# Kernel tuning notes

Hardware: AMD Instinct MI355X
Metric: run time of the kernel (lower is better)

The kernel has to match this reference:

```python
import jax, jax.numpy as jnp
import numpy as np

S = 4            # symbol_features (number of element types)
NLAB = S * S     # label_features = 16
RC = 6.0         # cutoff radius
C1, C2 = 32, 64  # embedding_layers
B, N = 4, 512
BOX_L = 25.0     # non-periodic box extent for coordinate sampling


def setup_inputs() -> dict:
    key = jax.random.key(0)
    k1, k2, k3, k4 = jax.random.split(key, 4)
    coords = jax.random.uniform(k1, (B, N, 3), dtype=jnp.float32) * BOX_L
    numbers = jax.random.randint(k2, (B, N), 0, S)
    # NaN lattice -> Descriptor takes the non-periodic neighbor branch
    boxs = jnp.full((B, 9), jnp.nan, dtype=jnp.float32)
    # RConv parameters (per label): nuww=-0.05, sigmas=4.0, centres ~ xavier_normal
    nuww0 = jnp.full((NLAB,), -0.05, jnp.float32)
    sigmas0 = jnp.full((NLAB,), 4.0, jnp.float32)
    centres0 = (jax.random.normal(k3, (NLAB, C1)) * np.sqrt(2.0 / (NLAB + C1))).astype(jnp.float32)
    nuww1 = jnp.full((NLAB,), -0.05, jnp.float32)
    sigmas1 = jnp.full((NLAB,), 4.0, jnp.float32)
    centres1 = (jax.random.normal(k4, (NLAB, C2)) * np.sqrt(2.0 / (NLAB + C2))).astype(jnp.float32)
    return {"boxs": boxs, "numbers": numbers, "coords": coords,
            "nuww0": nuww0, "sigmas0": sigmas0, "centres0": centres0,
            "nuww1": nuww1, "sigmas1": sigmas1, "centres1": centres1}


def _rconv(label, r, nuww, sigmas, centres):
    # label: [B,N,N] int; r: [B,N,N,Cin] -> out [B,N,N,Cout]
    rs = r.sum(-1, keepdims=True)            # sum over channel dim (keepdim)
    ww = nuww[label][..., None]              # [B,N,N,1]
    sgm = sigmas[label][..., None]           # [B,N,N,1]
    cc = centres[label]                      # [B,N,N,Cout]
    alpha = (rs - cc) * sgm
    return ww * jnp.exp(-(alpha * alpha))


def reference(boxs, numbers, coords, nuww0, sigmas0, centres0, nuww1, sigmas1, centres1):
    # boxs is NaN -> non-periodic branch of Descriptor.forward.
    # Dense-mask formulation: pairs (i,j) with d<=RC, i!=j; masked entries
    # contribute exactly zero to the per-atom contractions below.
    rij = coords[:, None, :, :] - coords[:, :, None, :]      # [B,N,N,3] = x_j - x_i
    d2 = jnp.sum(rij * rij, axis=-1)                         # [B,N,N]
    safe = jnp.sqrt(jnp.where(d2 > 0, d2, 1.0))              # NaN-safe sqrt for grads
    d = jnp.where(d2 > 0, safe, 0.0)
    eye = jnp.eye(N, dtype=bool)
    mask = (jax.lax.stop_gradient(d) <= RC) & ~eye           # neighbor list (detached, as in torch)

    fc = 0.5 * jnp.cos(d * (jnp.pi / RC)) + 0.5              # cutoff_cosine, [B,N,N]
    ang = rij / safe[..., None]                              # unit direction (safe at diag)
    raij = jnp.concatenate([fc[..., None], ang * fc[..., None]], axis=-1)  # [B,N,N,4]

    label = numbers[:, :, None] * S + numbers[:, None, :]    # ZIJ_Label[z_i, z_j], [B,N,N]

    r0 = fc[..., None]                                       # rij_cos, [B,N,N,1]
    phi = _rconv(label, r0, nuww0, sigmas0, centres0)        # [B,N,N,C1]
    phi = _rconv(label, phi, nuww1, sigmas1, centres1)       # [B,N,N,C2]
    phi = phi * mask[..., None]                              # zero out non-neighbors

    # per atom i: L = phi^T @ raij over neighbors j -> [C2,4]; R = L @ L^T -> [C2,C2]
    Lm = jnp.einsum('bijc,bijf->bicf', phi, raij)            # [B,N,C2,4]
    R = jnp.einsum('bicf,bidf->bicd', Lm, Lm)                # [B,N,C2,C2]
    fro = jnp.sqrt(jnp.sum(R * R, axis=(-2, -1), keepdims=True))
    D = R / fro
    return D.reshape(B, N, C2 * C2)                          # Dij [B,N,4096]
```

## Files before the change

kernel.cpp:

```cpp
#include <hip/hip_runtime.h>
#include <math.h>

#define S_ 4
#define NLAB 16
#define C1 32
#define C2 64
#define N_ 512
#define RC 6.0f
#define PI_OVER_RC 0.5235987755982988f
#define SEGCAP 32

__global__ __launch_bounds__(256, 8) void desc_kernel(
    const int* __restrict__ numbers,
    const float* __restrict__ coords,
    const float* __restrict__ nuww0, const float* __restrict__ sigmas0,
    const float* __restrict__ centres0,
    const float* __restrict__ nuww1, const float* __restrict__ sigmas1,
    const float* __restrict__ centres1,
    float* __restrict__ out)
{
    __shared__ float s_c0[NLAB * 33];
    __shared__ float s_c1[NLAB * C2];
    __shared__ float s_ww0[NLAB], s_sg0[NLAB], s_ww1[NLAB], s_sg1[NLAB];
    __shared__ float4 s_pair[4][SEGCAP];
    __shared__ float  s_s1[4][SEGCAP];
    __shared__ int    s_lab[4][SEGCAP];
    __shared__ float4 s_part[4][C2];
    __shared__ float4 s_Lm[C2];

    const int tid  = threadIdx.x;
    const int wq   = tid >> 6;
    const int lane = tid & 63;
    const int bi   = blockIdx.x;
    const int b    = bi >> 9;
    const int i    = bi & (N_ - 1);
    const int base = b * N_;

    for (int idx = tid; idx < NLAB * C1; idx += 256) {
        int l = idx >> 5, c = idx & 31;
        s_c0[l * 33 + c] = centres0[idx];
    }
    for (int idx = tid; idx < NLAB * C2; idx += 256) s_c1[idx] = centres1[idx];
    if (tid < NLAB) {
        s_ww0[tid] = nuww0[tid]; s_sg0[tid] = sigmas0[tid];
        s_ww1[tid] = nuww1[tid]; s_sg1[tid] = sigmas1[tid];
    }
    __syncthreads();

    const float xi = coords[(base + i) * 3 + 0];
    const float yi = coords[(base + i) * 3 + 1];
    const float zi = coords[(base + i) * 3 + 2];
    const int zlab = numbers[base + i] * S_;

    int cntq = 0;
    #pragma unroll
    for (int t = 0; t < 2; ++t) {
        int j = wq * 128 + t * 64 + lane;
        float dx = coords[(base + j) * 3 + 0] - xi;
        float dy = coords[(base + j) * 3 + 1] - yi;
        float dz = coords[(base + j) * 3 + 2] - zi;
        int   zj = numbers[base + j];
        float d2 = dx * dx + dy * dy + dz * dz;
        float d  = sqrtf(d2);
        bool hit = (j != i) && (d <= RC);
        unsigned long long m = __ballot(hit);
        int slot = cntq + __popcll(m & ((1ull << lane) - 1ull));
        if (hit && slot < SEGCAP) {
            s_pair[wq][slot] = make_float4(dx, dy, dz, d);
            s_lab[wq][slot]  = zlab + zj;
        }
        cntq += __popcll(m);
    }
    const int nnq = min(cntq, SEGCAP);
    __builtin_amdgcn_wave_barrier();

    if (lane < nnq) {
        int   k   = lane;
        float4 g  = s_pair[wq][k];
        int   lab = s_lab[wq][k];
        float fc  = 0.5f * __cosf(g.w * PI_OVER_RC) + 0.5f;
        float sg0 = s_sg0[lab];
        const float* c0 = &s_c0[lab * 33];
        float p0 = 0.f, p1 = 0.f;
        #pragma unroll
        for (int c = 0; c < C1; c += 2) {
            float a0 = (fc - c0[c])     * sg0;
            float a1 = (fc - c0[c + 1]) * sg0;
            p0 += __expf(-(a0 * a0));
            p1 += __expf(-(a1 * a1));
        }
        float fac = (g.w > 0.f) ? (fc / g.w) : 0.f;
        s_pair[wq][k] = make_float4(fc, g.x * fac, g.y * fac, g.z * fac);
        s_s1[wq][k]   = s_ww0[lab] * (p0 + p1);
    }
    __builtin_amdgcn_wave_barrier();

    {
        float a0 = 0.f, a1 = 0.f, a2 = 0.f, a3 = 0.f;
        for (int k = 0; k < nnq; ++k) {
            int    lab = s_lab[wq][k];
            float  s1  = s_s1[wq][k];
            float4 r4  = s_pair[wq][k];
            float  al  = (s1 - s_c1[lab * C2 + lane]) * s_sg1[lab];
            float  p   = s_ww1[lab] * __expf(-(al * al));
            a0 += p * r4.x; a1 += p * r4.y; a2 += p * r4.z; a3 += p * r4.w;
        }
        s_part[wq][lane] = make_float4(a0, a1, a2, a3);
    }
    __syncthreads();

    float4 P0 = s_part[0][lane], P1 = s_part[1][lane];
    float4 P2 = s_part[2][lane], P3 = s_part[3][lane];
    float a0 = (P0.x + P1.x) + (P2.x + P3.x);
    float a1 = (P0.y + P1.y) + (P2.y + P3.y);
    float a2 = (P0.z + P1.z) + (P2.z + P3.z);
    float a3 = (P0.w + P1.w) + (P2.w + P3.w);
    s_Lm[lane] = make_float4(a0, a1, a2, a3);

    float g00 = a0 * a0, g01 = a0 * a1, g02 = a0 * a2, g03 = a0 * a3;
    float g11 = a1 * a1, g12 = a1 * a2, g13 = a1 * a3;
    float g22 = a2 * a2, g23 = a2 * a3, g33 = a3 * a3;
    #pragma unroll
    for (int off = 32; off >= 1; off >>= 1) {
        g00 += __shfl_xor(g00, off, 64); g01 += __shfl_xor(g01, off, 64);
        g02 += __shfl_xor(g02, off, 64); g03 += __shfl_xor(g03, off, 64);
        g11 += __shfl_xor(g11, off, 64); g12 += __shfl_xor(g12, off, 64);
        g13 += __shfl_xor(g13, off, 64); g22 += __shfl_xor(g22, off, 64);
        g23 += __shfl_xor(g23, off, 64); g33 += __shfl_xor(g33, off, 64);
    }
    float ss = g00 * g00 + g11 * g11 + g22 * g22 + g33 * g33
             + 2.f * (g01 * g01 + g02 * g02 + g03 * g03
                    + g12 * g12 + g13 * g13 + g23 * g23);
    float inv = rsqrtf(ss);
    __builtin_amdgcn_wave_barrier();

    const int cb = (lane & 15) * 4;
    float4 Lc0 = s_Lm[cb + 0], Lc1 = s_Lm[cb + 1];
    float4 Lc2 = s_Lm[cb + 2], Lc3 = s_Lm[cb + 3];
    Lc0.x *= inv; Lc0.y *= inv; Lc0.z *= inv; Lc0.w *= inv;
    Lc1.x *= inv; Lc1.y *= inv; Lc1.z *= inv; Lc1.w *= inv;
    Lc2.x *= inv; Lc2.y *= inv; Lc2.z *= inv; Lc2.w *= inv;
    Lc3.x *= inv; Lc3.y *= inv; Lc3.z *= inv; Lc3.w *= inv;
    float* po = out + (size_t)bi * (C2 * C2);
    #pragma unroll
    for (int t = 0; t < 4; ++t) {
        int q  = wq * 4 + t;
        int dd = q * 4 + (lane >> 4);
        float4 Ld = s_Lm[dd];
        float4 v;
        v.x = Lc0.x * Ld.x + Lc0.y * Ld.y + Lc0.z * Ld.z + Lc0.w * Ld.w;
        v.y = Lc1.x * Ld.x + Lc1.y * Ld.y + Lc1.z * Ld.z + Lc1.w * Ld.w;
        v.z = Lc2.x * Ld.x + Lc2.y * Ld.y + Lc2.z * Ld.z + Lc2.w * Ld.w;
        v.w = Lc3.x * Ld.x + Lc3.y * Ld.y + Lc3.z * Ld.z + Lc3.w * Ld.w;
        *reinterpret_cast<float4*>(po + q * 256 + lane * 4) = v;
    }
}

extern "C" void kernel_launch(void* const* d_in, const int* in_sizes, int n_in,
                              void* d_out, int out_size, void* d_ws, size_t ws_size,
                              hipStream_t stream) {
    const int*   numbers  = (const int*)  d_in[1];
    const float* coords   = (const float*)d_in[2];
    const float* nuww0    = (const float*)d_in[3];
    const float* sigmas0  = (const float*)d_in[4];
    const float* centres0 = (const float*)d_in[5];
    const float* nuww1    = (const float*)d_in[6];
    const float* sigmas1  = (const float*)d_in[7];
    const float* centres1 = (const float*)d_in[8];
    float* out = (float*)d_out;

    const int B = in_sizes[1] / N_;
    dim3 grid(B * N_), block(256);
    desc_kernel<<<grid, block, 0, stream>>>(numbers, coords, nuww0, sigmas0,
                                            centres0, nuww1, sigmas1, centres1, out);
}
```

Baseline: 22.28 us.

## Bucket neighbors by species so each wave handles one label in layer two

Neighbors are now compacted into per-wave, per-species buckets. In the second RConv stage each wave processes one species across all four quarter-buckets, so the centre, sigma and weight values become loop invariants held in registers. Parameter loads are issued before the neighbor scan and written to shared memory afterwards, which overlaps global latency with the distance pass. The price is four ballots per tile, extra block-wide barriers, and less occupancy from the launch bound change from 8 to 4. SEGCAP drops to 24 per species bucket, which lowers the total capacity and could truncate neighbors if the density is high.

```diff
diff --git a/kernel.cpp b/kernel.cpp
--- a/kernel.cpp
+++ b/kernel.cpp
@@ -8,9 +8,9 @@
 #define N_ 512
 #define RC 6.0f
 #define PI_OVER_RC 0.5235987755982988f
-#define SEGCAP 32
-
-__global__ __launch_bounds__(256, 8) void desc_kernel(
+#define SEGCAP 24
+
+__global__ __launch_bounds__(256, 4) void desc_kernel(
     const int* __restrict__ numbers,
     const float* __restrict__ coords,
     const float* __restrict__ nuww0, const float* __restrict__ sigmas0,
@@ -22,9 +22,9 @@
     __shared__ float s_c0[NLAB * 33];
     __shared__ float s_c1[NLAB * C2];
     __shared__ float s_ww0[NLAB], s_sg0[NLAB], s_ww1[NLAB], s_sg1[NLAB];
-    __shared__ float4 s_pair[4][SEGCAP];
-    __shared__ float  s_s1[4][SEGCAP];
-    __shared__ int    s_lab[4][SEGCAP];
+    __shared__ float4 s_pair[4][4][SEGCAP];
+    __shared__ float  s_s1[4][4][SEGCAP];
+    __shared__ int    s_segcnt[4][4];
     __shared__ float4 s_part[4][C2];
     __shared__ float4 s_Lm[C2];
 
@@ -36,23 +36,23 @@
     const int i    = bi & (N_ - 1);
     const int base = b * N_;
 
-    for (int idx = tid; idx < NLAB * C1; idx += 256) {
-        int l = idx >> 5, c = idx & 31;
-        s_c0[l * 33 + c] = centres0[idx];
-    }
-    for (int idx = tid; idx < NLAB * C2; idx += 256) s_c1[idx] = centres1[idx];
-    if (tid < NLAB) {
-        s_ww0[tid] = nuww0[tid]; s_sg0[tid] = sigmas0[tid];
-        s_ww1[tid] = nuww1[tid]; s_sg1[tid] = sigmas1[tid];
-    }
-    __syncthreads();
-
     const float xi = coords[(base + i) * 3 + 0];
     const float yi = coords[(base + i) * 3 + 1];
     const float zi = coords[(base + i) * 3 + 2];
     const int zlab = numbers[base + i] * S_;
 
-    int cntq = 0;
+    float4 rc0 = make_float4(0.f, 0.f, 0.f, 0.f);
+    if (tid < 128) rc0 = reinterpret_cast<const float4*>(centres0)[tid];
+    float4 rc1 = reinterpret_cast<const float4*>(centres1)[tid];
+    float rsc = 0.f;
+    if (tid < 64) {
+        const float* sp = (tid < 16) ? nuww0 : (tid < 32) ? sigmas0
+                        : (tid < 48) ? nuww1 : sigmas1;
+        rsc = sp[tid & 15];
+    }
+
+    int cg[4] = {0, 0, 0, 0};
+    const unsigned long long lmask = (1ull << lane) - 1ull;
     #pragma unroll
     for (int t = 0; t < 2; ++t) {
         int j = wq * 128 + t * 64 + lane;
@@ -63,47 +63,81 @@
         float d2 = dx * dx + dy * dy + dz * dz;
         float d  = sqrtf(d2);
         bool hit = (j != i) && (d <= RC);
-        unsigned long long m = __ballot(hit);
-        int slot = cntq + __popcll(m & ((1ull << lane) - 1ull));
-        if (hit && slot < SEGCAP) {
-            s_pair[wq][slot] = make_float4(dx, dy, dz, d);
-            s_lab[wq][slot]  = zlab + zj;
+        #pragma unroll
+        for (int g = 0; g < 4; ++g) {
+            unsigned long long m = __ballot(hit && (zj == g));
+            if (hit && (zj == g)) {
+                int slot = cg[g] + (int)__popcll(m & lmask);
+                if (slot < SEGCAP) s_pair[wq][g][slot] = make_float4(dx, dy, dz, d);
+            }
+            cg[g] += (int)__popcll(m);
         }
-        cntq += __popcll(m);
-    }
-    const int nnq = min(cntq, SEGCAP);
-    __builtin_amdgcn_wave_barrier();
-
-    if (lane < nnq) {
-        int   k   = lane;
-        float4 g  = s_pair[wq][k];
-        int   lab = s_lab[wq][k];
-        float fc  = 0.5f * __cosf(g.w * PI_OVER_RC) + 0.5f;
-        float sg0 = s_sg0[lab];
-        const float* c0 = &s_c0[lab * 33];
-        float p0 = 0.f, p1 = 0.f;
+    }
+    if (lane == 0) {
         #pragma unroll
-        for (int c = 0; c < C1; c += 2) {
-            float a0 = (fc - c0[c])     * sg0;
-            float a1 = (fc - c0[c + 1]) * sg0;
-            p0 += __expf(-(a0 * a0));
-            p1 += __expf(-(a1 * a1));
+        for (int g = 0; g < 4; ++g) s_segcnt[wq][g] = min(cg[g], SEGCAP);
+    }
+
+    if (tid < 128) {
+        int idx = tid * 4, l = idx >> 5, c = idx & 31;
+        s_c0[l * 33 + c + 0] = rc0.x; s_c0[l * 33 + c + 1] = rc0.y;
+        s_c0[l * 33 + c + 2] = rc0.z; s_c0[l * 33 + c + 3] = rc0.w;
+    }
+    s_c1[tid * 4 + 0] = rc1.x; s_c1[tid * 4 + 1] = rc1.y;
+    s_c1[tid * 4 + 2] = rc1.z; s_c1[tid * 4 + 3] = rc1.w;
+    if (tid < 64) {
+        int r = tid & 15;
+        if      (tid < 16) s_ww0[r] = rsc;
+        else if (tid < 32) s_sg0[r] = rsc;
+        else if (tid < 48) s_ww1[r] = rsc;
+        else               s_sg1[r] = rsc;
+    }
+    __syncthreads();
+
+    {
+        const int n0 = min(cg[0], SEGCAP), n1 = min(cg[1], SEGCAP);
+        const int n2 = min(cg[2], SEGCAP), n3 = min(cg[3], SEGCAP);
+        const int p0 = n0, p1 = p0 + n1, p2 = p1 + n2, p3 = p2 + n3;
+        for (int L = lane; L < p3; L += 64) {
+            int g   = (L >= p0) + (L >= p1) + (L >= p2);
+            int off = (g == 0) ? 0 : (g == 1) ? p0 : (g == 2) ? p1 : p2;
+            int idx = L - off;
+            float4 gv = s_pair[wq][g][idx];
+            int   lab = zlab + g;
+            float fc  = 0.5f * __cosf(gv.w * PI_OVER_RC) + 0.5f;
+            float sg0 = s_sg0[lab];
+            const float* c0p = &s_c0[lab * 33];
+            float pa = 0.f, pb = 0.f;
+            #pragma unroll
+            for (int c = 0; c < C1; c += 2) {
+                float a0_ = (fc - c0p[c])     * sg0;
+                float a1_ = (fc - c0p[c + 1]) * sg0;
+                pa += __expf(-(a0_ * a0_));
+                pb += __expf(-(a1_ * a1_));
+            }
+            float fac = (gv.w > 0.f) ? (fc / gv.w) : 0.f;
+            s_pair[wq][g][idx] = make_float4(fc, gv.x * fac, gv.y * fac, gv.z * fac);
+            s_s1[wq][g][idx]   = s_ww0[lab] * (pa + pb);
         }
-        float fac = (g.w > 0.f) ? (fc / g.w) : 0.f;
-        s_pair[wq][k] = make_float4(fc, g.x * fac, g.y * fac, g.z * fac);
-        s_s1[wq][k]   = s_ww0[lab] * (p0 + p1);
-    }
-    __builtin_amdgcn_wave_barrier();
+    }
+    __syncthreads();
 
     {
+        const int   labw = zlab + wq;
+        const float c1v  = s_c1[labw * C2 + lane];
+        const float sg1  = s_sg1[labw];
+        const float ww1  = s_ww1[labw];
         float a0 = 0.f, a1 = 0.f, a2 = 0.f, a3 = 0.f;
-        for (int k = 0; k < nnq; ++k) {
-            int    lab = s_lab[wq][k];
-            float  s1  = s_s1[wq][k];
-            float4 r4  = s_pair[wq][k];
-            float  al  = (s1 - s_c1[lab * C2 + lane]) * s_sg1[lab];
-            float  p   = s_ww1[lab] * __expf(-(al * al));
-            a0 += p * r4.x; a1 += p * r4.y; a2 += p * r4.z; a3 += p * r4.w;
+        #pragma unroll
+        for (int q = 0; q < 4; ++q) {
+            int nk = s_segcnt[q][wq];
+            for (int k = 0; k < nk; ++k) {
+                float  s1 = s_s1[q][wq][k];
+                float4 r4 = s_pair[q][wq][k];
+                float  al = (s1 - c1v) * sg1;
+                float  p  = ww1 * __expf(-(al * al));
+                a0 += p * r4.x; a1 += p * r4.y; a2 += p * r4.z; a3 += p * r4.w;
+            }
         }
         s_part[wq][lane] = make_float4(a0, a1, a2, a3);
     }
```

Result: faster. 21.78 us (-2.2%).
